# Performance work log

Hardware: AMD Instinct MI355X
Metric: run time of the kernel (lower is better)

## Reference

```python
import jax, jax.numpy as jnp
import numpy as np

N, C_IN, C_OUT, H, W = 16, 256, 256, 32, 32
K = 9  # 3x3 kernel


def setup_inputs() -> dict:
    key = jax.random.key(0)
    k1, k2, k3 = jax.random.split(key, 3)
    x = jax.random.normal(k1, (N, C_IN, H, W), dtype=jnp.float32)
    # offsets as produced upstream from anchors: (N, H*W, 18)
    offset = jax.random.normal(k2, (N, H * W, 2 * K), dtype=jnp.float32)
    # DeformConv weight (no bias), kaiming-ish scale
    weight = jax.random.normal(k3, (C_OUT, C_IN, 3, 3), dtype=jnp.float32) * 0.02
    return {"x": x, "offset": offset, "weight": weight}


def _deform_conv3x3(x, offset_nchw, weight):
    """DeformConv v1, kernel 3x3, stride 1, padding 1, dilation 1,
    groups=1, deformable_groups=1, zero padding outside borders."""
    n, c, h, w = x.shape
    o = weight.shape[0]
    # offset channel layout: (dy_k, dx_k) pairs for k = 0..8
    off = offset_nchw.reshape(n, K, 2, h, w)
    dy = off[:, :, 0]  # (N,K,H,W)
    dx = off[:, :, 1]
    ky = (jnp.arange(K) // 3 - 1).astype(x.dtype)  # kernel row offsets -1,0,1
    kx = (jnp.arange(K) % 3 - 1).astype(x.dtype)
    base_y = jnp.arange(h, dtype=x.dtype)[None, None, :, None]
    base_x = jnp.arange(w, dtype=x.dtype)[None, None, None, :]
    py = base_y + ky[None, :, None, None] + dy  # (N,K,H,W) sample rows
    px = base_x + kx[None, :, None, None] + dx  # (N,K,H,W) sample cols

    y0 = jnp.floor(py)
    x0 = jnp.floor(px)
    ly = py - y0  # fractional parts
    lx = px - x0

    x_flat = x.reshape(n, c, h * w)

    def corner(yi, xi, wgt):
        valid = (yi >= 0) & (yi <= h - 1) & (xi >= 0) & (xi <= w - 1)
        yc = jnp.clip(yi, 0, h - 1).astype(jnp.int32)
        xc = jnp.clip(xi, 0, w - 1).astype(jnp.int32)
        idx = (yc * w + xc).reshape(n, K * h * w)
        g = jax.vmap(lambda xf, i: xf[:, i])(x_flat, idx)  # (N,C,K*H*W)
        wv = (wgt * valid.astype(x.dtype)).reshape(n, 1, K * h * w)
        return g * wv

    val = (corner(y0, x0, (1 - ly) * (1 - lx))
           + corner(y0, x0 + 1, (1 - ly) * lx)
           + corner(y0 + 1, x0, ly * (1 - lx))
           + corner(y0 + 1, x0 + 1, ly * lx))
    val = val.reshape(n, c, K, h, w)  # sampled im2col columns
    return jnp.einsum('nckhw,ock->nohw', val, weight.reshape(o, c, K))


def reference(x, offset, weight):
    n, _, h, w = x.shape
    assert h * w == offset.shape[1]
    # AdaptiveConv.forward: (N, HW, 18) -> (N, 18, H, W)
    offset_nchw = jnp.transpose(offset, (0, 2, 1)).reshape(n, 2 * K, h, w)
    return _deform_conv3x3(x, offset_nchw, weight)
```

## Files before the change

kernel.cpp:

```cpp
#include <hip/hip_runtime.h>

#define NB   16
#define CIN  256
#define COUT 256
#define HH   32
#define WW   32
#define HW   1024
#define KK   9
#define CK   2304

typedef __bf16 bf16x8 __attribute__((ext_vector_type(8)));
typedef float  f32x4  __attribute__((ext_vector_type(4)));

__device__ __forceinline__ unsigned short f2bf(float f) {
    unsigned int u = __float_as_uint(f);
    u += 0x7FFFu + ((u >> 16) & 1u);
    return (unsigned short)(u >> 16);
}
__device__ __forceinline__ float bfhi(unsigned int u) {
    return __uint_as_float(u & 0xFFFF0000u);
}
__device__ __forceinline__ float bflo(unsigned int u) {
    return __uint_as_float(u << 16);
}
__device__ __forceinline__ unsigned pk2(float lo, float hi) {
    unsigned r;
    asm("v_cvt_pk_bf16_f32 %0, %1, %2" : "=v"(r) : "v"(lo), "v"(hi));
    return r;
}

typedef const __attribute__((address_space(1))) void* gas_ptr;
typedef __attribute__((address_space(3))) void* las_ptr;

__device__ __forceinline__ void async16(const void* g, void* l) {
    __builtin_amdgcn_global_load_lds((gas_ptr)g, (las_ptr)l, 16, 0, 0);
}

#define SB() __builtin_amdgcn_sched_barrier(0)
#define SYNC() do { SB(); asm volatile("s_waitcnt lgkmcnt(0)" ::: "memory"); SB(); \
                    __builtin_amdgcn_s_barrier(); SB(); } while (0)

__global__ __launch_bounds__(256) void prep_kernel(const float* __restrict__ w,
                                                   unsigned short* __restrict__ wbf,
                                                   const float* __restrict__ x,
                                                   unsigned short* __restrict__ xtb) {
    __shared__ float lsbuf[64 * 65];
    const int t = threadIdx.x;

    if (blockIdx.x < 256) {
        const int o = blockIdx.x;
        const float* wo = w + (size_t)o * CK;
#pragma unroll
        for (int i = t; i < CK; i += 256) lsbuf[i] = wo[i];
        __syncthreads();
        unsigned short* dst = wbf + (size_t)o * CK;
#pragma unroll
        for (int i = t; i < CK; i += 256) {
            int k = i >> 8, c = i & 255;
            dst[i] = f2bf(lsbuf[c * KK + k]);
        }
        return;
    }

    float (*ls)[65] = (float(*)[65])lsbuf;
    const int id  = blockIdx.x - 256;
    const int c0  = (id & 3) << 6;
    const int hw0 = ((id >> 2) & 15) << 6;
    const int n   = id >> 6;
    {
        int c = t >> 2, q = t & 3;
        const float4* base = (const float4*)(x + ((size_t)(n * CIN + c0 + c)) * HW + hw0 + q * 16);
#pragma unroll
        for (int j = 0; j < 4; ++j) {
            float4 v = base[j];
            ls[c][q * 16 + j * 4 + 0] = v.x;
            ls[c][q * 16 + j * 4 + 1] = v.y;
            ls[c][q * 16 + j * 4 + 2] = v.z;
            ls[c][q * 16 + j * 4 + 3] = v.w;
        }
    }
    __syncthreads();
    {
        int hw = t >> 2, seg = (t & 3) * 16;
        unsigned int dw[8];
#pragma unroll
        for (int j = 0; j < 8; ++j) {
            float f0 = ls[seg + 2 * j][hw];
            float f1 = ls[seg + 2 * j + 1][hw];
            dw[j] = (unsigned)f2bf(f0) | ((unsigned)f2bf(f1) << 16);
        }
        uint4* dst = (uint4*)(xtb + ((size_t)(n * HW + hw0 + hw)) * CIN + c0 + seg);
        dst[0] = *(uint4*)&dw[0];
        dst[1] = *(uint4*)&dw[4];
    }
}

__global__ __launch_bounds__(512, 2) void fused_kernel(const unsigned short* __restrict__ wbf,
                                                       const unsigned short* __restrict__ xtb,
                                                       const float* __restrict__ off,
                                                       float* __restrict__ out) {
    __shared__ unsigned short As[3][256 * 64];
    __shared__ unsigned short Bs[2][64 * 64];

    const int tid  = threadIdx.x;
    const int wv   = tid >> 6;
    const int lane = tid & 63;
    const int quad = lane >> 4;
    const int l15  = lane & 15;

    const int hw_local = tid >> 3;
    const int seg      = tid & 7;

    const int id  = blockIdx.x;
    const int n   = ((id & 7) << 1) | ((id >> 3) & 1);
    const int hw0 = (id >> 4) * 64;

    const int hw = hw0 + hw_local;
    const int h  = hw >> 5, w = hw & 31;

    const int srow   = lane >> 3;
    const int schunk = (lane & 7) ^ (srow & 7);

    const uint4*  xb4  = (const uint4*)(xtb + (size_t)n * HW * CIN);
    const float2* offp = (const float2*)(off + ((size_t)n * HW + hw) * (2 * KK));

    f32x4 acc[2][4] = {};

    auto setup2 = [&](float2 o, int tapv, float* wg, int* ix) {
        float py = (float)(h + tapv / 3 - 1) + o.x;
        float px = (float)(w + tapv % 3 - 1) + o.y;
        float y0f = floorf(py), x0f = floorf(px);
        float ly = py - y0f, lx = px - x0f;
        int y0 = (int)y0f, x0 = (int)x0f;
#pragma unroll
        for (int c2 = 0; c2 < 4; ++c2) {
            int yy = y0 + (c2 >> 1);
            int xx = x0 + (c2 & 1);
            float wy = (c2 >> 1) ? ly : 1.0f - ly;
            float wx = (c2 & 1) ? lx : 1.0f - lx;
            bool v = (yy >= 0) && (yy < HH) && (xx >= 0) && (xx < WW);
            wg[c2] = v ? wy * wx : 0.0f;
            int yc = yy < 0 ? 0 : (yy > HH - 1 ? HH - 1 : yy);
            int xc = xx < 0 ? 0 : (xx > WW - 1 ? WW - 1 : xx);
            ix[c2] = yc * WW + xc;
        }
    };

    auto loadc = [&](uint4 cr[4], const int* ix, int q) {
#pragma unroll
        for (int c2 = 0; c2 < 4; ++c2)
            cr[c2] = xb4[(size_t)ix[c2] * 32 + q * 8 + seg];
    };

    auto dmaA = [&](int ai, int kblk) {
        const unsigned short* wsrc = wbf + (size_t)kblk * 64 + (size_t)srow * CK + schunk * 8;
        unsigned short* dst = &As[ai][0];
#pragma unroll
        for (int j = 0; j < 4; ++j) {
            int rb = wv * 32 + j * 8;
            async16(wsrc + (size_t)rb * CK, dst + rb * 64);
        }
    };

    auto lerpB = [&](int bi, const uint4 cr[4], const float* wg) {
        unsigned u0[4], u1[4], u2[4], u3[4];
        *(uint4*)u0 = cr[0]; *(uint4*)u1 = cr[1];
        *(uint4*)u2 = cr[2]; *(uint4*)u3 = cr[3];
        unsigned dw[4];
#pragma unroll
        for (int d = 0; d < 4; ++d) {
            float lo = wg[0] * bflo(u0[d]) + wg[1] * bflo(u1[d])
                     + wg[2] * bflo(u2[d]) + wg[3] * bflo(u3[d]);
            float hi = wg[0] * bfhi(u0[d]) + wg[1] * bfhi(u1[d])
                     + wg[2] * bfhi(u2[d]) + wg[3] * bfhi(u3[d]);
            dw[d] = pk2(lo, hi);
        }
        *(uint4*)&Bs[bi][hw_local * 64 + (seg ^ (hw_local & 7)) * 8] = *(uint4*)dw;
    };

    auto frag_read = [&](int ai, int bi, bf16x8 af[2][2], bf16x8 bfr[4][2]) {
        const unsigned short* Ap = &As[ai][0];
        const unsigned short* Bp = &Bs[bi][0];
#pragma unroll
        for (int mi = 0; mi < 2; ++mi)
#pragma unroll
            for (int hh = 0; hh < 2; ++hh) {
                int row = wv * 32 + mi * 16 + l15;
                int ch  = (hh * 4 + quad) ^ (row & 7);
                af[mi][hh] = *(const bf16x8*)(Ap + row * 64 + ch * 8);
            }
#pragma unroll
        for (int ni = 0; ni < 4; ++ni)
#pragma unroll
            for (int hh = 0; hh < 2; ++hh) {
                int row = ni * 16 + l15;
                int ch  = (hh * 4 + quad) ^ (row & 7);
                bfr[ni][hh] = *(const bf16x8*)(Bp + row * 64 + ch * 8);
            }
    };

    auto frag_mma = [&](bf16x8 af[2][2], bf16x8 bfr[4][2]) {
        __builtin_amdgcn_s_setprio(1);
#pragma unroll
        for (int mi = 0; mi < 2; ++mi)
#pragma unroll
            for (int ni = 0; ni < 4; ++ni) {
                acc[mi][ni] = __builtin_amdgcn_mfma_f32_16x16x32_bf16(af[mi][0], bfr[ni][0], acc[mi][ni], 0, 0, 0);
                acc[mi][ni] = __builtin_amdgcn_mfma_f32_16x16x32_bf16(af[mi][1], bfr[ni][1], acc[mi][ni], 0, 0, 0);
            }
        __builtin_amdgcn_s_setprio(0);
    };

    float wgc[4], wgn[4];
    int   ixc[4], ixn[4];
    uint4 crA[4], crB[4];
    {
        float2 o0 = offp[0];
        setup2(o0, 0, wgc, ixc);
        dmaA(0, 0);
        dmaA(1, 1);
        SB();
        loadc(crA, ixc, 0);
        loadc(crB, ixc, 1);
        SB();
        lerpB(0, crA, wgc);
        SYNC();
    }

    int i0 = 0;
#pragma unroll 1
    for (int tap = 0; tap < 9; ++tap) {
        const int i1 = (i0 == 2) ? 0 : i0 + 1;
        const int i2 = (i1 == 2) ? 0 : i1 + 1;
        const int kb = tap * 4;
        const bool more = (tap < 8);
        bf16x8 af[2][2], bfr[4][2];

        frag_read(i0, 0, af, bfr);
        SB();
        dmaA(i2, kb + 2);
        SB();
        lerpB(1, crB, wgc);
        SB();
        loadc(crA, ixc, 2);
        SB();
        frag_mma(af, bfr);
        SYNC();

        frag_read(i1, 1, af, bfr);
        SB();
        dmaA(i0, kb + 3);
        SB();
        lerpB(0, crA, wgc);
        SB();
        loadc(crB, ixc, 3);
        SB();
        frag_mma(af, bfr);
        SYNC();

        float2 onx = {};
        if (more) onx = offp[tap + 1];
        SB();
        frag_read(i2, 0, af, bfr);
        SB();
        if (more) dmaA(i1, kb + 4);
        SB();
        lerpB(1, crB, wgc);
        SB();
        if (more) { setup2(onx, tap + 1, wgn, ixn); loadc(crA, ixn, 0); }
        SB();
        frag_mma(af, bfr);
        SYNC();

        frag_read(i0, 1, af, bfr);
        SB();
        if (more) {
            dmaA(i2, kb + 5);
            SB();
            lerpB(0, crA, wgn);
            SB();
            loadc(crB, ixn, 1);
#pragma unroll
            for (int c2 = 0; c2 < 4; ++c2) { wgc[c2] = wgn[c2]; ixc[c2] = ixn[c2]; }
            SB();
            frag_mma(af, bfr);
            SYNC();
        } else {
            frag_mma(af, bfr);
        }
        i0 = i1;
    }

    float* opnt = out + (size_t)n * COUT * HW + hw0;
#pragma unroll
    for (int mi = 0; mi < 2; ++mi)
#pragma unroll
        for (int ni = 0; ni < 4; ++ni) {
            int col = ni * 16 + l15;
#pragma unroll
            for (int rr = 0; rr < 4; ++rr) {
                int row = wv * 32 + mi * 16 + quad * 4 + rr;
                opnt[(size_t)row * HW + col] = acc[mi][ni][rr];
            }
        }
}

extern "C" void kernel_launch(void* const* d_in, const int* in_sizes, int n_in,
                              void* d_out, int out_size, void* d_ws, size_t ws_size,
                              hipStream_t stream) {
    const float* x   = (const float*)d_in[0];
    const float* off = (const float*)d_in[1];
    const float* wt  = (const float*)d_in[2];
    float* out = (float*)d_out;

    unsigned short* wbf = (unsigned short*)d_ws;
    unsigned short* xtb = (unsigned short*)((char*)d_ws + 1179648);

    prep_kernel<<<1280, 256, 0, stream>>>(wt, wbf, x, xtb);
    fused_kernel<<<256, 512, 0, stream>>>(wbf, xtb, off, out);
}
```

Before: 112.7 us.

## Double K-step to 128 per stage, halving barriers in deformable conv pipeline

Restructures the fused deform-conv GEMM pipeline from four 64-wide K stages per tap with a triple-buffered weight tile to two 128-wide stages per tap with double buffering. Each stage now covers half a tap, and the bilinear gather loads 128 channels. Explicit vmcnt waits replace the implicit ordering of async loads. The aim is to cut the number of block barriers and per-stage overhead, at the cost of more LDS per block, more live registers, and a shallower prefetch depth.

```diff
diff --git a/kernel.cpp b/kernel.cpp
--- a/kernel.cpp
+++ b/kernel.cpp
@@ -39,6 +39,8 @@
 #define SB() __builtin_amdgcn_sched_barrier(0)
 #define SYNC() do { SB(); asm volatile("s_waitcnt lgkmcnt(0)" ::: "memory"); SB(); \
                     __builtin_amdgcn_s_barrier(); SB(); } while (0)
+#define VM8() do { SB(); asm volatile("s_waitcnt vmcnt(8)" ::: "memory"); SB(); } while (0)
+#define VM0() do { SB(); asm volatile("s_waitcnt vmcnt(0)" ::: "memory"); SB(); } while (0)
 
 __global__ __launch_bounds__(256) void prep_kernel(const float* __restrict__ w,
                                                    unsigned short* __restrict__ wbf,
@@ -99,8 +101,8 @@
                                                        const unsigned short* __restrict__ xtb,
                                                        const float* __restrict__ off,
                                                        float* __restrict__ out) {
-    __shared__ unsigned short As[3][256 * 64];
-    __shared__ unsigned short Bs[2][64 * 64];
+    __shared__ unsigned short As[2][256 * 128];
+    __shared__ unsigned short Bs[2][64 * 128];
 
     const int tid  = threadIdx.x;
     const int wv   = tid >> 6;
@@ -109,7 +111,7 @@
     const int l15  = lane & 15;
 
     const int hw_local = tid >> 3;
-    const int seg      = tid & 7;
+    const int seg8     = tid & 7;
 
     const int id  = blockIdx.x;
     const int n   = ((id & 7) << 1) | ((id >> 3) & 1);
@@ -118,8 +120,8 @@
     const int hw = hw0 + hw_local;
     const int h  = hw >> 5, w = hw & 31;
 
-    const int srow   = lane >> 3;
-    const int schunk = (lane & 7) ^ (srow & 7);
+    const int srow4   = lane >> 4;
+    const int schunk  = lane & 15;
 
     const uint4*  xb4  = (const uint4*)(xtb + (size_t)n * HW * CIN);
     const float2* offp = (const float2*)(off + ((size_t)n * HW + hw) * (2 * KK));
@@ -146,39 +148,48 @@
         }
     };
 
-    auto loadc = [&](uint4 cr[4], const int* ix, int q) {
-#pragma unroll
-        for (int c2 = 0; c2 < 4; ++c2)
-            cr[c2] = xb4[(size_t)ix[c2] * 32 + q * 8 + seg];
-    };
-
-    auto dmaA = [&](int ai, int kblk) {
-        const unsigned short* wsrc = wbf + (size_t)kblk * 64 + (size_t)srow * CK + schunk * 8;
+    auto loadc = [&](uint4 cr[2][4], const int* ix, int hf) {
+#pragma unroll
+        for (int c2 = 0; c2 < 4; ++c2) {
+            size_t b = (size_t)ix[c2] * 32 + hf * 16 + seg8 * 2;
+            cr[0][c2] = xb4[b];
+            cr[1][c2] = xb4[b + 1];
+        }
+    };
+
+    auto dmaA = [&](int ai, int s) {
         unsigned short* dst = &As[ai][0];
-#pragma unroll
-        for (int j = 0; j < 4; ++j) {
-            int rb = wv * 32 + j * 8;
-            async16(wsrc + (size_t)rb * CK, dst + rb * 64);
-        }
-    };
-
-    auto lerpB = [&](int bi, const uint4 cr[4], const float* wg) {
-        unsigned u0[4], u1[4], u2[4], u3[4];
-        *(uint4*)u0 = cr[0]; *(uint4*)u1 = cr[1];
-        *(uint4*)u2 = cr[2]; *(uint4*)u3 = cr[3];
-        unsigned dw[4];
-#pragma unroll
-        for (int d = 0; d < 4; ++d) {
-            float lo = wg[0] * bflo(u0[d]) + wg[1] * bflo(u1[d])
-                     + wg[2] * bflo(u2[d]) + wg[3] * bflo(u3[d]);
-            float hi = wg[0] * bfhi(u0[d]) + wg[1] * bfhi(u1[d])
-                     + wg[2] * bfhi(u2[d]) + wg[3] * bfhi(u3[d]);
-            dw[d] = pk2(lo, hi);
-        }
-        *(uint4*)&Bs[bi][hw_local * 64 + (seg ^ (hw_local & 7)) * 8] = *(uint4*)dw;
-    };
-
-    auto frag_read = [&](int ai, int bi, bf16x8 af[2][2], bf16x8 bfr[4][2]) {
+        const unsigned short* wsrc = wbf + s * 128;
+#pragma unroll
+        for (int j = 0; j < 8; ++j) {
+            int rb  = wv * 32 + j * 4;
+            int row = rb + srow4;
+            async16(wsrc + (size_t)row * CK + ((schunk ^ (row & 7)) * 8),
+                    dst + rb * 128);
+        }
+    };
+
+    auto lerpB = [&](int bi, const uint4 cr[2][4], const float* wg) {
+#pragma unroll
+        for (int p = 0; p < 2; ++p) {
+            unsigned u0[4], u1[4], u2[4], u3[4];
+            *(uint4*)u0 = cr[p][0]; *(uint4*)u1 = cr[p][1];
+            *(uint4*)u2 = cr[p][2]; *(uint4*)u3 = cr[p][3];
+            unsigned dw[4];
+#pragma unroll
+            for (int d = 0; d < 4; ++d) {
+                float lo = wg[0] * bflo(u0[d]) + wg[1] * bflo(u1[d])
+                         + wg[2] * bflo(u2[d]) + wg[3] * bflo(u3[d]);
+                float hi = wg[0] * bfhi(u0[d]) + wg[1] * bfhi(u1[d])
+                         + wg[2] * bfhi(u2[d]) + wg[3] * bfhi(u3[d]);
+                dw[d] = pk2(lo, hi);
+            }
+            int c16 = seg8 * 2 + p;
+            *(uint4*)&Bs[bi][hw_local * 128 + ((c16 ^ (hw_local & 7)) * 8)] = *(uint4*)dw;
+        }
+    };
+
+    auto frag_read = [&](int ai, int bi, int h0, bf16x8 af[2][2], bf16x8 bfr[4][2]) {
         const unsigned short* Ap = &As[ai][0];
         const unsigned short* Bp = &Bs[bi][0];
 #pragma unroll
@@ -186,16 +197,16 @@
 #pragma unroll
             for (int hh = 0; hh < 2; ++hh) {
                 int row = wv * 32 + mi * 16 + l15;
-                int ch  = (hh * 4 + quad) ^ (row & 7);
-                af[mi][hh] = *(const bf16x8*)(Ap + row * 64 + ch * 8);
+                int ch  = ((h0 * 2 + hh) * 4 + quad) ^ (row & 7);
+                af[mi][hh] = *(const bf16x8*)(Ap + row * 128 + ch * 8);
             }
 #pragma unroll
         for (int ni = 0; ni < 4; ++ni)
 #pragma unroll
             for (int hh = 0; hh < 2; ++hh) {
                 int row = ni * 16 + l15;
-                int ch  = (hh * 4 + quad) ^ (row & 7);
-                bfr[ni][hh] = *(const bf16x8*)(Bp + row * 64 + ch * 8);
+                int ch  = ((h0 * 2 + hh) * 4 + quad) ^ (row & 7);
+                bfr[ni][hh] = *(const bf16x8*)(Bp + row * 128 + ch * 8);
             }
     };
 
@@ -213,82 +224,63 @@
 
     float wgc[4], wgn[4];
     int   ixc[4], ixn[4];
-    uint4 crA[4], crB[4];
+    uint4 crEv[2][4], crOd[2][4];
+    float2 offv;
     {
         float2 o0 = offp[0];
         setup2(o0, 0, wgc, ixc);
         dmaA(0, 0);
-        dmaA(1, 1);
-        SB();
-        loadc(crA, ixc, 0);
-        loadc(crB, ixc, 1);
-        SB();
-        lerpB(0, crA, wgc);
+        SB();
+        loadc(crEv, ixc, 0);
+        SB();
+        lerpB(0, crEv, wgc);
+        SB();
+        loadc(crOd, ixc, 1);
+        offv = offp[1];
         SYNC();
     }
 
-    int i0 = 0;
 #pragma unroll 1
-    for (int tap = 0; tap < 9; ++tap) {
-        const int i1 = (i0 == 2) ? 0 : i0 + 1;
-        const int i2 = (i1 == 2) ? 0 : i1 + 1;
-        const int kb = tap * 4;
-        const bool more = (tap < 8);
+    for (int t = 0; t < 9; ++t) {
         bf16x8 af[2][2], bfr[4][2];
 
-        frag_read(i0, 0, af, bfr);
-        SB();
-        dmaA(i2, kb + 2);
-        SB();
-        lerpB(1, crB, wgc);
-        SB();
-        loadc(crA, ixc, 2);
+        VM8();
+        frag_read(0, 0, 0, af, bfr);
+        SB();
+        dmaA(1, 2 * t + 1);
+        SB();
+        if (t < 8) setup2(offv, t + 1, wgn, ixn);
+        SB();
+        lerpB(1, crOd, wgc);
+        SB();
+        if (t < 8) loadc(crEv, ixn, 0);
+        SB();
+        frag_mma(af, bfr);
+        frag_read(0, 0, 1, af, bfr);
         SB();
         frag_mma(af, bfr);
         SYNC();
 
-        frag_read(i1, 1, af, bfr);
-        SB();
-        dmaA(i0, kb + 3);
-        SB();
-        lerpB(0, crA, wgc);
-        SB();
-        loadc(crB, ixc, 3);
+        if (t < 8) { VM8(); } else { VM0(); }
+        frag_read(1, 1, 0, af, bfr);
+        SB();
+        if (t < 7) offv = offp[t + 2];
+        SB();
+        if (t < 8) dmaA(0, 2 * t + 2);
+        SB();
+        if (t < 8) lerpB(0, crEv, wgn);
+        SB();
+        if (t < 8) loadc(crOd, ixn, 1);
         SB();
         frag_mma(af, bfr);
-        SYNC();
-
-        float2 onx = {};
-        if (more) onx = offp[tap + 1];
-        SB();
-        frag_read(i2, 0, af, bfr);
-        SB();
-        if (more) dmaA(i1, kb + 4);
-        SB();
-        lerpB(1, crB, wgc);
-        SB();
-        if (more) { setup2(onx, tap + 1, wgn, ixn); loadc(crA, ixn, 0); }
+        frag_read(1, 1, 1, af, bfr);
         SB();
         frag_mma(af, bfr);
-        SYNC();
-
-        frag_read(i0, 1, af, bfr);
-        SB();
-        if (more) {
-            dmaA(i2, kb + 5);
-            SB();
-            lerpB(0, crA, wgn);
-            SB();
-            loadc(crB, ixn, 1);
-#pragma unroll
-            for (int c2 = 0; c2 < 4; ++c2) { wgc[c2] = wgn[c2]; ixc[c2] = ixn[c2]; }
-            SB();
-            frag_mma(af, bfr);
+        if (t < 8) {
+#pragma unroll
+            for (int c2 = 0; c2 < 4; ++c2) wgc[c2] = wgn[c2];
             SYNC();
-        } else {
-            frag_mma(af, bfr);
-        }
-        i0 = i1;
+        }
     }
 
     float* opnt = out + (size_t)n * COUT * HW + hw0;
```

New measurement: 116.5 us. +3.3%, slower.

## Load weight fragments directly from global into registers instead of LDS staging

Applied to the files above, without the earlier changes.

Drops the triple-buffered LDS staging of the bf16 weight tile through async global-to-LDS DMA. Each wave now loads its A fragments straight from global memory into registers, double-buffered one k-block ahead. This removes 96 KB of LDS per block, which may allow more resident blocks, and cuts LDS traffic. In exchange each lane does uncoalesced 16-byte global reads spread across rows of stride CK, and those loads sit on the MFMA critical path with only one stage of prefetch.

```diff
diff --git a/kernel.cpp b/kernel.cpp
--- a/kernel.cpp
+++ b/kernel.cpp
@@ -29,13 +29,6 @@
     return r;
 }
 
-typedef const __attribute__((address_space(1))) void* gas_ptr;
-typedef __attribute__((address_space(3))) void* las_ptr;
-
-__device__ __forceinline__ void async16(const void* g, void* l) {
-    __builtin_amdgcn_global_load_lds((gas_ptr)g, (las_ptr)l, 16, 0, 0);
-}
-
 #define SB() __builtin_amdgcn_sched_barrier(0)
 #define SYNC() do { SB(); asm volatile("s_waitcnt lgkmcnt(0)" ::: "memory"); SB(); \
                     __builtin_amdgcn_s_barrier(); SB(); } while (0)
@@ -99,7 +92,6 @@
                                                        const unsigned short* __restrict__ xtb,
                                                        const float* __restrict__ off,
                                                        float* __restrict__ out) {
-    __shared__ unsigned short As[3][256 * 64];
     __shared__ unsigned short Bs[2][64 * 64];
 
     const int tid  = threadIdx.x;
@@ -117,9 +109,6 @@
 
     const int hw = hw0 + hw_local;
     const int h  = hw >> 5, w = hw & 31;
-
-    const int srow   = lane >> 3;
-    const int schunk = (lane & 7) ^ (srow & 7);
 
     const uint4*  xb4  = (const uint4*)(xtb + (size_t)n * HW * CIN);
     const float2* offp = (const float2*)(off + ((size_t)n * HW + hw) * (2 * KK));
@@ -152,14 +141,14 @@
             cr[c2] = xb4[(size_t)ix[c2] * 32 + q * 8 + seg];
     };
 
-    auto dmaA = [&](int ai, int kblk) {
-        const unsigned short* wsrc = wbf + (size_t)kblk * 64 + (size_t)srow * CK + schunk * 8;
-        unsigned short* dst = &As[ai][0];
-#pragma unroll
-        for (int j = 0; j < 4; ++j) {
-            int rb = wv * 32 + j * 8;
-            async16(wsrc + (size_t)rb * CK, dst + rb * 64);
-        }
+    auto loadA = [&](bf16x8 af[2][2], int s) {
+#pragma unroll
+        for (int mi = 0; mi < 2; ++mi)
+#pragma unroll
+            for (int hh = 0; hh < 2; ++hh) {
+                int row = wv * 32 + mi * 16 + l15;
+                af[mi][hh] = *(const bf16x8*)(wbf + (size_t)row * CK + s * 64 + (hh * 4 + quad) * 8);
+            }
     };
 
     auto lerpB = [&](int bi, const uint4 cr[4], const float* wg) {
@@ -178,17 +167,8 @@
         *(uint4*)&Bs[bi][hw_local * 64 + (seg ^ (hw_local & 7)) * 8] = *(uint4*)dw;
     };
 
-    auto frag_read = [&](int ai, int bi, bf16x8 af[2][2], bf16x8 bfr[4][2]) {
-        const unsigned short* Ap = &As[ai][0];
+    auto frag_readB = [&](int bi, bf16x8 bfr[4][2]) {
         const unsigned short* Bp = &Bs[bi][0];
-#pragma unroll
-        for (int mi = 0; mi < 2; ++mi)
-#pragma unroll
-            for (int hh = 0; hh < 2; ++hh) {
-                int row = wv * 32 + mi * 16 + l15;
-                int ch  = (hh * 4 + quad) ^ (row & 7);
-                af[mi][hh] = *(const bf16x8*)(Ap + row * 64 + ch * 8);
-            }
 #pragma unroll
         for (int ni = 0; ni < 4; ++ni)
 #pragma unroll
@@ -214,68 +194,66 @@
     float wgc[4], wgn[4];
     int   ixc[4], ixn[4];
     uint4 crA[4], crB[4];
+    bf16x8 afA[2][2], afB[2][2];
     {
         float2 o0 = offp[0];
         setup2(o0, 0, wgc, ixc);
-        dmaA(0, 0);
-        dmaA(1, 1);
+        loadA(afA, 0);
         SB();
         loadc(crA, ixc, 0);
+        SB();
+        lerpB(0, crA, wgc);
+        SB();
         loadc(crB, ixc, 1);
-        SB();
-        lerpB(0, crA, wgc);
-        SYNC();
-    }
-
-    int i0 = 0;
+        SYNC();
+    }
+
 #pragma unroll 1
     for (int tap = 0; tap < 9; ++tap) {
-        const int i1 = (i0 == 2) ? 0 : i0 + 1;
-        const int i2 = (i1 == 2) ? 0 : i1 + 1;
         const int kb = tap * 4;
         const bool more = (tap < 8);
-        bf16x8 af[2][2], bfr[4][2];
-
-        frag_read(i0, 0, af, bfr);
-        SB();
-        dmaA(i2, kb + 2);
+        bf16x8 bfr[4][2];
+
+        frag_readB(0, bfr);
+        SB();
+        loadA(afB, kb + 1);
         SB();
         lerpB(1, crB, wgc);
         SB();
         loadc(crA, ixc, 2);
         SB();
-        frag_mma(af, bfr);
-        SYNC();
-
-        frag_read(i1, 1, af, bfr);
-        SB();
-        dmaA(i0, kb + 3);
+        frag_mma(afA, bfr);
+        SYNC();
+
+        frag_readB(1, bfr);
+        SB();
+        loadA(afA, kb + 2);
         SB();
         lerpB(0, crA, wgc);
         SB();
         loadc(crB, ixc, 3);
         SB();
-        frag_mma(af, bfr);
+        frag_mma(afB, bfr);
         SYNC();
 
         float2 onx = {};
         if (more) onx = offp[tap + 1];
         SB();
-        frag_read(i2, 0, af, bfr);
-        SB();
-        if (more) dmaA(i1, kb + 4);
+        frag_readB(0, bfr);
+        SB();
+        loadA(afB, kb + 3);
         SB();
         lerpB(1, crB, wgc);
         SB();
         if (more) { setup2(onx, tap + 1, wgn, ixn); loadc(crA, ixn, 0); }
         SB();
-        frag_mma(af, bfr);
-        SYNC();
-
-        frag_read(i0, 1, af, bfr);
+        frag_mma(afA, bfr);
+        SYNC();
+
+        frag_readB(1, bfr);
         SB();
         if (more) {
-            dmaA(i2, kb + 5);
+            loadA(afA, kb + 4);
             SB();
             lerpB(0, crA, wgn);
             SB();
@@ -283,12 +261,11 @@
 #pragma unroll
             for (int c2 = 0; c2 < 4; ++c2) { wgc[c2] = wgn[c2]; ixc[c2] = ixn[c2]; }
             SB();
-            frag_mma(af, bfr);
+            frag_mma(afB, bfr);
             SYNC();
         } else {
-            frag_mma(af, bfr);
-        }
-        i0 = i1;
+            frag_mma(afB, bfr);
+        }
     }
 
     float* opnt = out + (size_t)n * COUT * HW + hw0;
```

Measured after the change: 120.8 us. 7.2% more time.

## Restructure deform-conv pipeline to two K-chunks per barrier with 4-stage buffers

Applied to the files above, without the earlier changes.

Switches the fused kernel's main loop from a 3-deep A ring and 2-deep B ring, with one barrier per 64-wide K chunk, to 4 A and 4 B LDS buffers processed two chunks per barrier. Explicit vmcnt waits replace the implicit ordering, and offset loads and bilinear setup are hoisted one tap ahead. The goal is to halve the barrier count and give gathers and DMA more time to land before use. LDS grows to about 160KB, which at 512 threads and launch bounds of 2 may cut occupancy to one block per CU, and the vmcnt thresholds have to match the number of outstanding loads exactly.

```diff
diff --git a/kernel.cpp b/kernel.cpp
--- a/kernel.cpp
+++ b/kernel.cpp
@@ -39,6 +39,8 @@
 #define SB() __builtin_amdgcn_sched_barrier(0)
 #define SYNC() do { SB(); asm volatile("s_waitcnt lgkmcnt(0)" ::: "memory"); SB(); \
                     __builtin_amdgcn_s_barrier(); SB(); } while (0)
+#define VM8() do { SB(); asm volatile("s_waitcnt vmcnt(8)" ::: "memory"); SB(); } while (0)
+#define VM0() do { SB(); asm volatile("s_waitcnt vmcnt(0)" ::: "memory"); SB(); } while (0)
 
 __global__ __launch_bounds__(256) void prep_kernel(const float* __restrict__ w,
                                                    unsigned short* __restrict__ wbf,
@@ -99,8 +101,8 @@
                                                        const unsigned short* __restrict__ xtb,
                                                        const float* __restrict__ off,
                                                        float* __restrict__ out) {
-    __shared__ unsigned short As[3][256 * 64];
-    __shared__ unsigned short Bs[2][64 * 64];
+    __shared__ unsigned short As[4][256 * 64];
+    __shared__ unsigned short Bs[4][64 * 64];
 
     const int tid  = threadIdx.x;
     const int wv   = tid >> 6;
@@ -213,7 +215,8 @@
 
     float wgc[4], wgn[4];
     int   ixc[4], ixn[4];
-    uint4 crA[4], crB[4];
+    uint4 crA[4], crB[4], crC[4], crD[4];
+    float2 offv;
     {
         float2 o0 = offp[0];
         setup2(o0, 0, wgc, ixc);
@@ -224,71 +227,68 @@
         loadc(crB, ixc, 1);
         SB();
         lerpB(0, crA, wgc);
+        lerpB(1, crB, wgc);
+        SB();
+        loadc(crC, ixc, 2);
+        loadc(crD, ixc, 3);
+        offv = offp[1];
         SYNC();
     }
 
-    int i0 = 0;
 #pragma unroll 1
-    for (int tap = 0; tap < 9; ++tap) {
-        const int i1 = (i0 == 2) ? 0 : i0 + 1;
-        const int i2 = (i1 == 2) ? 0 : i1 + 1;
-        const int kb = tap * 4;
-        const bool more = (tap < 8);
+    for (int t = 0; t < 9; ++t) {
+        const int kb = t * 4;
+        const bool more = (t < 8);
         bf16x8 af[2][2], bfr[4][2];
 
-        frag_read(i0, 0, af, bfr);
-        SB();
-        dmaA(i2, kb + 2);
-        SB();
-        lerpB(1, crB, wgc);
-        SB();
-        loadc(crA, ixc, 2);
+        VM8();
+        frag_read(0, 0, af, bfr);
+        SB();
+        dmaA(2, kb + 2);
+        dmaA(3, kb + 3);
+        SB();
+        if (more) setup2(offv, t + 1, wgn, ixn);
+        SB();
+        lerpB(2, crC, wgc);
+        lerpB(3, crD, wgc);
+        SB();
+        frag_mma(af, bfr);
+        SB();
+        frag_read(1, 1, af, bfr);
+        SB();
+        if (more) {
+            loadc(crA, ixn, 0);
+            loadc(crB, ixn, 1);
+        }
         SB();
         frag_mma(af, bfr);
         SYNC();
 
-        frag_read(i1, 1, af, bfr);
-        SB();
-        dmaA(i0, kb + 3);
-        SB();
-        lerpB(0, crA, wgc);
-        SB();
-        loadc(crB, ixc, 3);
-        SB();
-        frag_mma(af, bfr);
-        SYNC();
-
-        float2 onx = {};
-        if (more) onx = offp[tap + 1];
-        SB();
-        frag_read(i2, 0, af, bfr);
-        SB();
-        if (more) dmaA(i1, kb + 4);
-        SB();
-        lerpB(1, crB, wgc);
-        SB();
-        if (more) { setup2(onx, tap + 1, wgn, ixn); loadc(crA, ixn, 0); }
-        SB();
-        frag_mma(af, bfr);
-        SYNC();
-
-        frag_read(i0, 1, af, bfr);
+        if (more) { VM8(); } else { VM0(); }
+        frag_read(2, 2, af, bfr);
         SB();
         if (more) {
-            dmaA(i2, kb + 5);
+            dmaA(0, kb + 4);
+            dmaA(1, kb + 5);
             SB();
             lerpB(0, crA, wgn);
-            SB();
-            loadc(crB, ixn, 1);
-#pragma unroll
-            for (int c2 = 0; c2 < 4; ++c2) { wgc[c2] = wgn[c2]; ixc[c2] = ixn[c2]; }
-            SB();
-            frag_mma(af, bfr);
-            SYNC();
-        } else {
-            frag_mma(af, bfr);
-        }
-        i0 = i1;
+            lerpB(1, crB, wgn);
+        }
+        SB();
+        frag_mma(af, bfr);
+        SB();
+        frag_read(3, 3, af, bfr);
+        SB();
+        if (more) {
+            loadc(crC, ixn, 2);
+            loadc(crD, ixn, 3);
+            if (t < 7) offv = offp[t + 2];
+#pragma unroll
+            for (int c2 = 0; c2 < 4; ++c2) wgc[c2] = wgn[c2];
+        }
+        SB();
+        frag_mma(af, bfr);
+        if (more) SYNC();
     }
 
     float* opnt = out + (size_t)n * COUT * HW + hw0;
```

New measurement: 115.5 us. 2.4% more time.
